# Performance work log

Hardware: AMD Instinct MI355X
Metric: run time of the kernel (lower is better)

## Reference

```python
import jax, jax.numpy as jnp
import numpy as np

BINS = 64
EPS = 1e-8


def _compute_histogram(gray, bins=BINS):
    # gray: [B, H, W] -> normalized histogram [B, bins]
    B = gray.shape[0]
    flat = gray.reshape(B, -1)                      # [B, N]
    mn = flat.min(axis=1, keepdims=True)
    mx = flat.max(axis=1, keepdims=True)
    valid = mx > mn                                  # [B, 1]
    norm = (flat - mn) / jnp.where(valid, mx - mn, 1.0)
    idx = jnp.clip((norm * (bins - 1)).astype(jnp.int32), 0, bins - 1)  # [B, N]
    # per-image bincount via scatter-add
    hist = jax.vmap(lambda i: jnp.zeros(bins, dtype=flat.dtype).at[i].add(1.0))(idx)
    hist = hist / hist.sum(axis=1, keepdims=True)
    return jnp.where(valid, hist, jnp.full_like(hist, 1.0 / bins))


def reference(x, y, lambda_cc=10.0):
    # channel balance
    x_mean = jnp.mean(x, axis=(2, 3), keepdims=True)   # [B,3,1,1]
    y_mean = jnp.mean(y, axis=(2, 3), keepdims=True)
    x_bal = x_mean / (jnp.sum(x_mean, axis=1, keepdims=True) + EPS)
    y_bal = y_mean / (jnp.sum(y_mean, axis=1, keepdims=True) + EPS)
    color_balance_loss = jnp.mean(jnp.abs(x_bal - y_bal))

    # luminance
    x_gray = 0.299 * x[:, 0] + 0.587 * x[:, 1] + 0.114 * x[:, 2]  # [B,H,W]
    y_gray = 0.299 * y[:, 0] + 0.587 * y[:, 1] + 0.114 * y[:, 2]

    x_hist = _compute_histogram(x_gray)
    y_hist = _compute_histogram(y_gray)

    # F.kl_div(log(x_hist+eps), y_hist, reduction='batchmean')
    log_in = jnp.log(x_hist + EPS)
    ylogy = jnp.where(y_hist > 0, y_hist * jnp.log(jnp.where(y_hist > 0, y_hist, 1.0)), 0.0)
    kl = jnp.sum(ylogy - y_hist * log_in) / x.shape[0]

    return lambda_cc * (color_balance_loss + kl)


def setup_inputs() -> dict:
    key = jax.random.key(0)
    k1, k2 = jax.random.split(key)
    x = jax.random.uniform(k1, (16, 3, 512, 512), dtype=jnp.float32)
    y = jax.random.uniform(k2, (16, 3, 512, 512), dtype=jnp.float32)
    return {"x": x, "y": y}
```

## Files before the change

### kernel.cpp

```cpp
#include <hip/hip_runtime.h>

#define HW_N (512 * 512)
#define BINS 64
#define BPI  128
#define TPB  256
#define QPB  ((HW_N / 4) / BPI)
#define MAXB 16

struct Part {
    double sum[6];
    float  mn[2];
    float  mx[2];
};

__device__ __forceinline__ unsigned int f2ord(float f) {
    unsigned int u = __float_as_uint(f);
    return (u & 0x80000000u) ? ~u : (u | 0x80000000u);
}

__device__ __forceinline__ float grayf(float r, float g, float b) {
    return 0.299f * r + 0.587f * g + 0.114f * b;
}

__device__ __forceinline__ double waveSumD(double v) {
#pragma unroll
    for (int o = 32; o > 0; o >>= 1) v += __shfl_down(v, o);
    return v;
}
__device__ __forceinline__ float waveMinAll(float v) {
#pragma unroll
    for (int o = 32; o > 0; o >>= 1) v = fminf(v, __shfl_xor(v, o));
    return v;
}
__device__ __forceinline__ float waveMaxAll(float v) {
#pragma unroll
    for (int o = 32; o > 0; o >>= 1) v = fmaxf(v, __shfl_xor(v, o));
    return v;
}

__global__ __launch_bounds__(TPB) void k_pass1(const float* __restrict__ x,
                                               const float* __restrict__ y,
                                               Part* __restrict__ part,
                                               unsigned int* __restrict__ img_hist) {
    const int tid = threadIdx.x;
    const int blk = blockIdx.x;
    const int b   = blk / BPI;
    const int sub = blk % BPI;

    if (sub == 0)
        for (int i = tid; i < 2 * BINS; i += TPB) img_hist[b * 2 * BINS + i] = 0u;

    const int q0 = sub * QPB;
    const size_t base = (size_t)b * 3 * HW_N;

    const float4* xr = (const float4*)(x + base);
    const float4* xg = (const float4*)(x + base + HW_N);
    const float4* xb = (const float4*)(x + base + 2 * HW_N);
    const float4* yr = (const float4*)(y + base);
    const float4* yg = (const float4*)(y + base + HW_N);
    const float4* yb = (const float4*)(y + base + 2 * HW_N);

    float s0 = 0.f, s1 = 0.f, s2 = 0.f;
    float t0 = 0.f, t1 = 0.f, t2 = 0.f;
    float mnx = 3.4e38f, mxx = -3.4e38f;
    float mny = 3.4e38f, mxy = -3.4e38f;

    for (int i = tid; i < QPB; i += TPB) {
        const int q = q0 + i;
        float4 r = xr[q], g = xg[q], bl = xb[q];
        s0 += (r.x + r.y) + (r.z + r.w);
        s1 += (g.x + g.y) + (g.z + g.w);
        s2 += (bl.x + bl.y) + (bl.z + bl.w);
        {
            float g0 = grayf(r.x, g.x, bl.x), g1 = grayf(r.y, g.y, bl.y);
            float g2 = grayf(r.z, g.z, bl.z), g3 = grayf(r.w, g.w, bl.w);
            mnx = fminf(mnx, fminf(fminf(g0, g1), fminf(g2, g3)));
            mxx = fmaxf(mxx, fmaxf(fmaxf(g0, g1), fmaxf(g2, g3)));
        }
        r = yr[q]; g = yg[q]; bl = yb[q];
        t0 += (r.x + r.y) + (r.z + r.w);
        t1 += (g.x + g.y) + (g.z + g.w);
        t2 += (bl.x + bl.y) + (bl.z + bl.w);
        {
            float g0 = grayf(r.x, g.x, bl.x), g1 = grayf(r.y, g.y, bl.y);
            float g2 = grayf(r.z, g.z, bl.z), g3 = grayf(r.w, g.w, bl.w);
            mny = fminf(mny, fminf(fminf(g0, g1), fminf(g2, g3)));
            mxy = fmaxf(mxy, fmaxf(fmaxf(g0, g1), fmaxf(g2, g3)));
        }
    }

    const int wave = tid >> 6;
    const int lane = tid & 63;
    __shared__ double shs[6][TPB / 64];
    __shared__ float  shmn[2][TPB / 64];
    __shared__ float  shmx[2][TPB / 64];

    double d;
    d = waveSumD((double)s0); if (!lane) shs[0][wave] = d;
    d = waveSumD((double)s1); if (!lane) shs[1][wave] = d;
    d = waveSumD((double)s2); if (!lane) shs[2][wave] = d;
    d = waveSumD((double)t0); if (!lane) shs[3][wave] = d;
    d = waveSumD((double)t1); if (!lane) shs[4][wave] = d;
    d = waveSumD((double)t2); if (!lane) shs[5][wave] = d;
    float f;
    f = waveMinAll(mnx); if (!lane) shmn[0][wave] = f;
    f = waveMinAll(mny); if (!lane) shmn[1][wave] = f;
    f = waveMaxAll(mxx); if (!lane) shmx[0][wave] = f;
    f = waveMaxAll(mxy); if (!lane) shmx[1][wave] = f;
    __syncthreads();

    if (tid == 0) {
        Part& p = part[blk];
        p.sum[0] = shs[0][0] + shs[0][1] + shs[0][2] + shs[0][3];
        p.sum[1] = shs[1][0] + shs[1][1] + shs[1][2] + shs[1][3];
        p.sum[2] = shs[2][0] + shs[2][1] + shs[2][2] + shs[2][3];
        p.sum[3] = shs[3][0] + shs[3][1] + shs[3][2] + shs[3][3];
        p.sum[4] = shs[4][0] + shs[4][1] + shs[4][2] + shs[4][3];
        p.sum[5] = shs[5][0] + shs[5][1] + shs[5][2] + shs[5][3];
        p.mn[0] = fminf(fminf(shmn[0][0], shmn[0][1]), fminf(shmn[0][2], shmn[0][3]));
        p.mn[1] = fminf(fminf(shmn[1][0], shmn[1][1]), fminf(shmn[1][2], shmn[1][3]));
        p.mx[0] = fmaxf(fmaxf(shmx[0][0], shmx[0][1]), fmaxf(shmx[0][2], shmx[0][3]));
        p.mx[1] = fmaxf(fmaxf(shmx[1][0], shmx[1][1]), fmaxf(shmx[1][2], shmx[1][3]));
    }
}

__global__ __launch_bounds__(TPB) void k_pass2(const float* __restrict__ x,
                                               const float* __restrict__ y,
                                               const Part* __restrict__ part,
                                               unsigned int* __restrict__ img_hist) {
    const int tid = threadIdx.x;
    const int blk = blockIdx.x;
    const int b   = blk / BPI;
    const int sub = blk % BPI;
    const int wave = tid >> 6;
    const int lane = tid & 63;

    const Part* pb = part + (size_t)b * BPI;
    const float4 m0 = *(const float4*)&pb[lane].mn[0];
    const float4 m1 = *(const float4*)&pb[lane + 64].mn[0];
    const float imnx = waveMinAll(fminf(m0.x, m1.x));
    const float imny = waveMinAll(fminf(m0.y, m1.y));
    const float imxx = waveMaxAll(fmaxf(m0.z, m1.z));
    const float imxy = waveMaxAll(fmaxf(m0.w, m1.w));
    const float rgx = (imxx > imnx) ? (imxx - imnx) : 1.0f;
    const float rgy = (imxy > imny) ? (imxy - imny) : 1.0f;

    __shared__ unsigned int lh[8][BINS];
    for (int i = tid; i < 8 * BINS; i += TPB) ((unsigned int*)lh)[i] = 0u;
    __syncthreads();

    const int q0 = sub * QPB;
    const size_t base = (size_t)b * 3 * HW_N;
    const float4* xr = (const float4*)(x + base);
    const float4* xg = (const float4*)(x + base + HW_N);
    const float4* xb = (const float4*)(x + base + 2 * HW_N);
    const float4* yr = (const float4*)(y + base);
    const float4* yg = (const float4*)(y + base + HW_N);
    const float4* yb = (const float4*)(y + base + 2 * HW_N);

    unsigned int* hx = lh[wave];
    unsigned int* hy = lh[4 + wave];

    for (int i = tid; i < QPB; i += TPB) {
        const int q = q0 + i;
        float4 r = xr[q], g = xg[q], bl = xb[q];
        {
            float gv[4] = { grayf(r.x, g.x, bl.x), grayf(r.y, g.y, bl.y),
                            grayf(r.z, g.z, bl.z), grayf(r.w, g.w, bl.w) };
#pragma unroll
            for (int j = 0; j < 4; j++) {
                float t = ((gv[j] - imnx) / rgx) * 63.0f;
                int id = (int)t;
                id = id < 0 ? 0 : (id > 63 ? 63 : id);
                atomicAdd(&hx[id], 1u);
            }
        }
        r = yr[q]; g = yg[q]; bl = yb[q];
        {
            float gv[4] = { grayf(r.x, g.x, bl.x), grayf(r.y, g.y, bl.y),
                            grayf(r.z, g.z, bl.z), grayf(r.w, g.w, bl.w) };
#pragma unroll
            for (int j = 0; j < 4; j++) {
                float t = ((gv[j] - imny) / rgy) * 63.0f;
                int id = (int)t;
                id = id < 0 ? 0 : (id > 63 ? 63 : id);
                atomicAdd(&hy[id], 1u);
            }
        }
    }
    __syncthreads();

    for (int i = tid; i < 2 * BINS; i += TPB) {
        const int src = i >> 6, bin = i & 63;
        unsigned int v = lh[src * 4 + 0][bin] + lh[src * 4 + 1][bin] +
                         lh[src * 4 + 2][bin] + lh[src * 4 + 3][bin];
        if (v) atomicAdd(&img_hist[(b * 2 + src) * BINS + bin], v);
    }
}

__global__ __launch_bounds__(1024) void k_final(const Part* __restrict__ part,
                                                const unsigned int* __restrict__ img_hist,
                                                float* __restrict__ out, int B) {
    const int tid = threadIdx.x;

    __shared__ double ssum[MAXB][6];
    __shared__ unsigned int somn[MAXB][2], somx[MAXB][2];
    __shared__ double skl[16], scb[16];

    for (int t = tid; t < B * 6; t += 1024) {
        const int bb = t / 6, k = t - bb * 6;
        double a = 0.0;
#pragma unroll 8
        for (int s = 0; s < BPI; s++) a += part[bb * BPI + s].sum[k];
        ssum[bb][k] = a;
    }
    for (int t = tid; t < MAXB * 2; t += 1024) {
        somn[t >> 1][t & 1] = 0xFFFFFFFFu;
        somx[t >> 1][t & 1] = 0u;
    }
    __syncthreads();
    for (int t = tid; t < B * BPI; t += 1024) {
        const int bb = t / BPI;
        const float4 mm = *(const float4*)&part[t].mn[0];
        atomicMin(&somn[bb][0], f2ord(mm.x));
        atomicMin(&somn[bb][1], f2ord(mm.y));
        atomicMax(&somx[bb][0], f2ord(mm.z));
        atomicMax(&somx[bb][1], f2ord(mm.w));
    }
    __syncthreads();

    const float invN = 1.0f / (float)HW_N;
    double klt = 0.0, cbt = 0.0;

    for (int t = tid; t < B * BINS; t += 1024) {
        const int bb = t >> 6, bin = t & 63;
        const bool vldx = somx[bb][0] > somn[bb][0];
        const bool vldy = somx[bb][1] > somn[bb][1];
        const float xh = vldx ? (float)img_hist[(bb * 2 + 0) * BINS + bin] * invN : (1.0f / BINS);
        const float yh = vldy ? (float)img_hist[(bb * 2 + 1) * BINS + bin] * invN : (1.0f / BINS);
        const float log_in = logf(xh + 1e-8f);
        const float ylogy = (yh > 0.0f) ? yh * logf(yh) : 0.0f;
        klt += (double)ylogy - (double)yh * (double)log_in;
    }

    for (int t = tid; t < B * 3; t += 1024) {
        const int bb = t / 3, c = t - bb * 3;
        const double N = (double)HW_N;
        const double xbal = (ssum[bb][c] / N) /
                            ((ssum[bb][0] + ssum[bb][1] + ssum[bb][2]) / N + 1e-8);
        const double ybal = (ssum[bb][3 + c] / N) /
                            ((ssum[bb][3] + ssum[bb][4] + ssum[bb][5]) / N + 1e-8);
        cbt += fabs(xbal - ybal);
    }

    const double kw = waveSumD(klt);
    const double cw = waveSumD(cbt);
    const int wave = tid >> 6, lane = tid & 63;
    if (!lane) { skl[wave] = kw; scb[wave] = cw; }
    __syncthreads();
    if (tid == 0) {
        double K = 0.0, C = 0.0;
        for (int i = 0; i < 16; i++) { K += skl[i]; C += scb[i]; }
        const double kl = K / (double)B;
        const double cb = C / (double)(B * 3);
        out[0] = (float)(10.0 * (cb + kl));
    }
}

extern "C" void kernel_launch(void* const* d_in, const int* in_sizes, int n_in,
                              void* d_out, int out_size, void* d_ws, size_t ws_size,
                              hipStream_t stream) {
    const float* x = (const float*)d_in[0];
    const float* y = (const float*)d_in[1];
    float* out = (float*)d_out;
    const int B = in_sizes[0] / (3 * HW_N);

    Part* part = (Part*)d_ws;
    unsigned int* img_hist =
        (unsigned int*)((char*)d_ws + (size_t)B * BPI * sizeof(Part));

    k_pass1<<<B * BPI, TPB, 0, stream>>>(x, y, part, img_hist);
    k_pass2<<<B * BPI, TPB, 0, stream>>>(x, y, part, img_hist);
    k_final<<<1, 1024, 0, stream>>>(part, img_hist, out, B);
}
```

Baseline: 151.0 us.

## Materialize grayscale in pass1 so pass2 reads one plane instead of three

Pass1 now writes the computed luminance for x and y to workspace buffers, and pass2 builds its histograms from these single-channel buffers instead of re-reading all three RGB channels. This replaces re-reading the six input planes with one extra write and a read of two gray planes. Blocks per image are halved, which coarsens the work per block and changes the min/max partial reduction to one entry per lane. It depends on the workspace being large enough for two full gray images per batch.

Result: faster. 142.7 us (-5.5%).

```diff
diff --git a/kernel.cpp b/kernel.cpp
--- a/kernel.cpp
+++ b/kernel.cpp
@@ -2,7 +2,7 @@
 
 #define HW_N (512 * 512)
 #define BINS 64
-#define BPI  128
+#define BPI  64
 #define TPB  256
 #define QPB  ((HW_N / 4) / BPI)
 #define MAXB 16
@@ -41,7 +41,9 @@
 __global__ __launch_bounds__(TPB) void k_pass1(const float* __restrict__ x,
                                                const float* __restrict__ y,
                                                Part* __restrict__ part,
-                                               unsigned int* __restrict__ img_hist) {
+                                               unsigned int* __restrict__ img_hist,
+                                               float* __restrict__ gx,
+                                               float* __restrict__ gy) {
     const int tid = threadIdx.x;
     const int blk = blockIdx.x;
     const int b   = blk / BPI;
@@ -59,6 +61,8 @@
     const float4* yr = (const float4*)(y + base);
     const float4* yg = (const float4*)(y + base + HW_N);
     const float4* yb = (const float4*)(y + base + 2 * HW_N);
+    float4* gxp = (float4*)(gx + (size_t)b * HW_N);
+    float4* gyp = (float4*)(gy + (size_t)b * HW_N);
 
     float s0 = 0.f, s1 = 0.f, s2 = 0.f;
     float t0 = 0.f, t1 = 0.f, t2 = 0.f;
@@ -76,6 +80,7 @@
             float g2 = grayf(r.z, g.z, bl.z), g3 = grayf(r.w, g.w, bl.w);
             mnx = fminf(mnx, fminf(fminf(g0, g1), fminf(g2, g3)));
             mxx = fmaxf(mxx, fmaxf(fmaxf(g0, g1), fmaxf(g2, g3)));
+            gxp[q] = make_float4(g0, g1, g2, g3);
         }
         r = yr[q]; g = yg[q]; bl = yb[q];
         t0 += (r.x + r.y) + (r.z + r.w);
@@ -86,6 +91,7 @@
             float g2 = grayf(r.z, g.z, bl.z), g3 = grayf(r.w, g.w, bl.w);
             mny = fminf(mny, fminf(fminf(g0, g1), fminf(g2, g3)));
             mxy = fmaxf(mxy, fmaxf(fmaxf(g0, g1), fmaxf(g2, g3)));
+            gyp[q] = make_float4(g0, g1, g2, g3);
         }
     }
 
@@ -124,8 +130,8 @@
     }
 }
 
-__global__ __launch_bounds__(TPB) void k_pass2(const float* __restrict__ x,
-                                               const float* __restrict__ y,
+__global__ __launch_bounds__(TPB) void k_pass2(const float* __restrict__ gx,
+                                               const float* __restrict__ gy,
                                                const Part* __restrict__ part,
                                                unsigned int* __restrict__ img_hist) {
     const int tid = threadIdx.x;
@@ -135,13 +141,11 @@
     const int wave = tid >> 6;
     const int lane = tid & 63;
 
-    const Part* pb = part + (size_t)b * BPI;
-    const float4 m0 = *(const float4*)&pb[lane].mn[0];
-    const float4 m1 = *(const float4*)&pb[lane + 64].mn[0];
-    const float imnx = waveMinAll(fminf(m0.x, m1.x));
-    const float imny = waveMinAll(fminf(m0.y, m1.y));
-    const float imxx = waveMaxAll(fmaxf(m0.z, m1.z));
-    const float imxy = waveMaxAll(fmaxf(m0.w, m1.w));
+    const float4 mm = *(const float4*)&part[b * BPI + lane].mn[0];
+    const float imnx = waveMinAll(mm.x);
+    const float imny = waveMinAll(mm.y);
+    const float imxx = waveMaxAll(mm.z);
+    const float imxy = waveMaxAll(mm.w);
     const float rgx = (imxx > imnx) ? (imxx - imnx) : 1.0f;
     const float rgy = (imxy > imny) ? (imxy - imny) : 1.0f;
 
@@ -150,38 +154,31 @@
     __syncthreads();
 
     const int q0 = sub * QPB;
-    const size_t base = (size_t)b * 3 * HW_N;
-    const float4* xr = (const float4*)(x + base);
-    const float4* xg = (const float4*)(x + base + HW_N);
-    const float4* xb = (const float4*)(x + base + 2 * HW_N);
-    const float4* yr = (const float4*)(y + base);
-    const float4* yg = (const float4*)(y + base + HW_N);
-    const float4* yb = (const float4*)(y + base + 2 * HW_N);
+    const float4* gxp = (const float4*)(gx + (size_t)b * HW_N);
+    const float4* gyp = (const float4*)(gy + (size_t)b * HW_N);
 
     unsigned int* hx = lh[wave];
     unsigned int* hy = lh[4 + wave];
 
     for (int i = tid; i < QPB; i += TPB) {
         const int q = q0 + i;
-        float4 r = xr[q], g = xg[q], bl = xb[q];
-        {
-            float gv[4] = { grayf(r.x, g.x, bl.x), grayf(r.y, g.y, bl.y),
-                            grayf(r.z, g.z, bl.z), grayf(r.w, g.w, bl.w) };
+        {
+            const float4 gv = gxp[q];
+            const float g[4] = { gv.x, gv.y, gv.z, gv.w };
 #pragma unroll
             for (int j = 0; j < 4; j++) {
-                float t = ((gv[j] - imnx) / rgx) * 63.0f;
+                float t = ((g[j] - imnx) / rgx) * 63.0f;
                 int id = (int)t;
                 id = id < 0 ? 0 : (id > 63 ? 63 : id);
                 atomicAdd(&hx[id], 1u);
             }
         }
-        r = yr[q]; g = yg[q]; bl = yb[q];
-        {
-            float gv[4] = { grayf(r.x, g.x, bl.x), grayf(r.y, g.y, bl.y),
-                            grayf(r.z, g.z, bl.z), grayf(r.w, g.w, bl.w) };
+        {
+            const float4 gv = gyp[q];
+            const float g[4] = { gv.x, gv.y, gv.z, gv.w };
 #pragma unroll
             for (int j = 0; j < 4; j++) {
-                float t = ((gv[j] - imny) / rgy) * 63.0f;
+                float t = ((g[j] - imny) / rgy) * 63.0f;
                 int id = (int)t;
                 id = id < 0 ? 0 : (id > 63 ? 63 : id);
                 atomicAdd(&hy[id], 1u);
@@ -275,11 +272,13 @@
     float* out = (float*)d_out;
     const int B = in_sizes[0] / (3 * HW_N);
 
-    Part* part = (Part*)d_ws;
-    unsigned int* img_hist =
-        (unsigned int*)((char*)d_ws + (size_t)B * BPI * sizeof(Part));
-
-    k_pass1<<<B * BPI, TPB, 0, stream>>>(x, y, part, img_hist);
-    k_pass2<<<B * BPI, TPB, 0, stream>>>(x, y, part, img_hist);
+    char* ws = (char*)d_ws;
+    Part* part = (Part*)ws;
+    unsigned int* img_hist = (unsigned int*)(ws + (size_t)B * BPI * sizeof(Part));
+    float* gx = (float*)(ws + (1 << 20));
+    float* gy = gx + (size_t)B * HW_N;
+
+    k_pass1<<<B * BPI, TPB, 0, stream>>>(x, y, part, img_hist, gx, gy);
+    k_pass2<<<B * BPI, TPB, 0, stream>>>(gx, gy, part, img_hist);
     k_final<<<1, 1024, 0, stream>>>(part, img_hist, out, B);
 }
```
